# Kernel tuning notes

Measured on AMD Instinct MI355X. Metric: run time of the kernel, lower is better.

The kernel has to match this reference:

```python
import jax, jax.numpy as jnp
import numpy as np

B, S, H, E, K, F = 2, 2048, 1024, 8, 2, 4096


def setup_inputs() -> dict:
    key = jax.random.key(0)
    ks = jax.random.split(key, 6)
    scale = 0.02
    return {
        "x": jax.random.normal(ks[0], (B, S, H), dtype=jnp.float32),
        "Wg": jax.random.normal(ks[1], (H, E), dtype=jnp.float32) * scale,
        "bg": jnp.zeros((E,), dtype=jnp.float32),
        "W1": jax.random.normal(ks[2], (E, H, F), dtype=jnp.float32) * scale,  # gate proj per expert
        "W3": jax.random.normal(ks[3], (E, H, F), dtype=jnp.float32) * scale,  # up proj per expert
        "W2": jax.random.normal(ks[4], (E, F, H), dtype=jnp.float32) * scale,  # down proj per expert
    }


def reference(x, Wg, bg, W1, W3, W2):
    # --- gating: softmax -> top-k -> renormalize ---
    probs = jax.nn.softmax(jnp.einsum("bsh,he->bse", x, Wg) + bg, axis=-1)  # [B,S,E]
    topw, topi = jax.lax.top_k(probs, K)                                     # [B,S,K]
    topw = topw / jnp.sum(topw, axis=-1, keepdims=True)
    # combine weights per expert: sum over k slots of weight where index==e
    cw = jnp.sum(jax.nn.one_hot(topi, E, dtype=x.dtype) * topw[..., None], axis=-2)  # [B,S,E]

    # --- dense grouped SwiGLU experts; cw==0 zeroes out non-selected tokens,
    # which is mathematically identical to the original masked gather/scatter loop ---
    g = jnp.einsum("bsh,ehf->bsef", x, W1)            # [B,S,E,F]
    u = jnp.einsum("bsh,ehf->bsef", x, W3)            # [B,S,E,F]
    h = jax.nn.silu(g) * u                             # [B,S,E,F]
    out = jnp.einsum("bsef,efh,bse->bsh", h, W2, cw)  # weighted combine
    return out
```

## Files before the change

### kernel.cpp

```cpp
#include <hip/hip_runtime.h>
#include <hip/hip_bf16.h>
#include <math.h>

#define HD 1024
#define FD 4096
#define NE 8
#define CAP 4096

typedef __attribute__((ext_vector_type(8))) short short8;
typedef __attribute__((ext_vector_type(4))) float f32x4;

__device__ inline unsigned short f2b(float f) {
    union { float f; unsigned u; } v; v.f = f;
    unsigned r = v.u + 0x7FFF + ((v.u >> 16) & 1);
    return (unsigned short)(r >> 16);
}

__device__ inline void gll16(const void* g, void* l) {
    __builtin_amdgcn_global_load_lds(
        (const __attribute__((address_space(1))) unsigned int*)g,
        (__attribute__((address_space(3))) unsigned int*)l, 16, 0, 0);
}

__global__ __launch_bounds__(256) void convx_kernel(const float* __restrict__ x,
                                                    unsigned short* __restrict__ xbf)
{
    int i = blockIdx.x * 256 + threadIdx.x;
    float4 v = *(const float4*)(x + (size_t)i * 4);
    ushort4 b; b.x = f2b(v.x); b.y = f2b(v.y); b.z = f2b(v.z); b.w = f2b(v.w);
    *(ushort4*)(xbf + (size_t)i * 4) = b;
}

__global__ __launch_bounds__(256) void transpose_kernel(const float* __restrict__ in,
                                                        unsigned short* __restrict__ out,
                                                        int R, int C)
{
    __shared__ unsigned short Ls[64 * 72];
    int t = threadIdx.x;
    int r0 = blockIdx.x * 64, c0 = blockIdx.y * 64;
    const float* ip = in + (size_t)blockIdx.z * R * C;
    unsigned short* op = out + (size_t)blockIdx.z * (size_t)R * C;

    int rl = t >> 4, c4 = (t & 15) * 4;
#pragma unroll
    for (int p = 0; p < 4; p++) {
        int r = p * 16 + rl;
        float4 v = *(const float4*)(ip + (size_t)(r0 + r) * C + c0 + c4);
        Ls[(c4 + 0) * 72 + r] = f2b(v.x);
        Ls[(c4 + 1) * 72 + r] = f2b(v.y);
        Ls[(c4 + 2) * 72 + r] = f2b(v.z);
        Ls[(c4 + 3) * 72 + r] = f2b(v.w);
    }
    __syncthreads();
    int c = t >> 2, j2 = (t & 3) * 2;
    int orow = c0 + c;
    int blk = orow >> 7, rl2 = orow & 127;
#pragma unroll
    for (int q = 0; q < 2; q++) {
        int j = j2 + q;
        int kk = r0 + j * 8;
        uint4 v = *(const uint4*)&Ls[c * 72 + j * 8];
        size_t dst = (size_t)blk * 128 * R + (size_t)(kk >> 5) * 4096 + rl2 * 32 + (kk & 31);
        *(uint4*)(op + dst) = v;
    }
}

__global__ __launch_bounds__(256) void gate_kernel(
    const float* __restrict__ x, const float* __restrict__ Wg,
    const float* __restrict__ bg, int* __restrict__ cnt,
    int* __restrict__ btok, float* __restrict__ bw,
    int* __restrict__ tokSlot, int T)
{
    int wave = threadIdx.x >> 6;
    int lane = threadIdx.x & 63;
    int t = blockIdx.x * 4 + wave;
    if (t >= T) return;

    float part[NE];
#pragma unroll
    for (int e = 0; e < NE; e++) part[e] = 0.f;
    const float* xr = x + (size_t)t * HD;
#pragma unroll 4
    for (int j = 0; j < 16; j++) {
        int h = lane + 64 * j;
        float xv = xr[h];
        const float* wr = Wg + h * NE;
#pragma unroll
        for (int e = 0; e < NE; e++) part[e] += xv * wr[e];
    }
#pragma unroll
    for (int e = 0; e < NE; e++) {
        float v = part[e];
        for (int off = 32; off >= 1; off >>= 1) v += __shfl_xor(v, off, 64);
        part[e] = v;
    }
    if (lane == 0) {
        float lg[NE];
#pragma unroll
        for (int e = 0; e < NE; e++) lg[e] = part[e] + bg[e];
        int i0 = 0;
        for (int e = 1; e < NE; e++) if (lg[e] > lg[i0]) i0 = e;
        int i1 = -1;
        for (int e = 0; e < NE; e++) {
            if (e == i0) continue;
            if (i1 < 0 || lg[e] > lg[i1]) i1 = e;
        }
        float e1 = expf(lg[i1] - lg[i0]);
        float s = 1.0f + e1;
        float w0 = 1.0f / s, w1 = e1 / s;
        int p0 = atomicAdd(&cnt[i0], 1);
        int p1 = atomicAdd(&cnt[i1], 1);
        btok[i0 * CAP + p0] = t; bw[i0 * CAP + p0] = w0;
        btok[i1 * CAP + p1] = t; bw[i1 * CAP + p1] = w1;
        tokSlot[t * 2 + 0] = i0 * CAP + p0;
        tokSlot[t * 2 + 1] = i1 * CAP + p1;
    }
}

__global__ void scan_kernel(const int* __restrict__ cnt, int* __restrict__ offs)
{
    if (threadIdx.x == 0) {
        int acc = 0;
        for (int e = 0; e < NE; e++) { offs[e] = acc; acc += cnt[e]; }
    }
}

__global__ __launch_bounds__(256, 2) void gemm1_kernel(
    const unsigned short* __restrict__ xbf, const unsigned short* __restrict__ Wt1,
    const unsigned short* __restrict__ Wt3, const int* __restrict__ btok,
    const int* __restrict__ cnt, const int* __restrict__ offs,
    unsigned short* __restrict__ h_buf)
{
    int e = blockIdx.z;
    int ne = cnt[e];
    int m0 = blockIdx.y * 128;
    if (m0 >= ne) return;
    int f0 = blockIdx.x * 128;

    __shared__ unsigned short As[3][4096];
    __shared__ unsigned short B1s[3][4096];
    __shared__ unsigned short B3s[3][4096];

    int tid = threadIdx.x;
    int lane = tid & 63;
    int w = tid >> 6;
    int wm = (w >> 1) * 64, wn = (w & 1) * 64;
    int l15 = lane & 15, quad = lane >> 4;

    const unsigned short* W1e = Wt1 + (size_t)e * HD * FD + (size_t)blockIdx.x * (128 * HD);
    const unsigned short* W3e = Wt3 + (size_t)e * HD * FD + (size_t)blockIdx.x * (128 * HD);

    const unsigned short* aA[2];
    const unsigned short* aB1[2];
    const unsigned short* aB3[2];
    int dst[2];
#pragma unroll
    for (int q = 0; q < 2; q++) {
        int g = w * 2 + q;
        int row = g * 16 + (lane >> 2);
        int cofs = (lane & 3) * 8;
        dst[q] = g * 512;
        int ridx = m0 + row; if (ridx >= ne) ridx = ne - 1;
        int tok = btok[e * CAP + ridx];
        aA[q]  = xbf + (size_t)tok * HD + cofs;
        aB1[q] = W1e + g * 512 + lane * 8;
        aB3[q] = W3e + g * 512 + lane * 8;
    }

    int aoff[4], boff[4];
#pragma unroll
    for (int i = 0; i < 4; i++) {
        aoff[i] = (wm + i * 16 + l15) * 32 + quad * 8;
        boff[i] = (wn + i * 16 + l15) * 32 + quad * 8;
    }

    f32x4 accG[4][4], accU[4][4];
    f32x4 z = {0.f, 0.f, 0.f, 0.f};
#pragma unroll
    for (int i = 0; i < 4; i++)
#pragma unroll
        for (int jj = 0; jj < 4; jj++) { accG[i][jj] = z; accU[i][jj] = z; }

#pragma unroll
    for (int q = 0; q < 2; q++) {
        gll16(aA[q],  &As[0][dst[q]]);
        gll16(aB1[q], &B1s[0][dst[q]]);
        gll16(aB3[q], &B3s[0][dst[q]]);
    }
#pragma unroll
    for (int q = 0; q < 2; q++) {
        gll16(aA[q]  + 32,   &As[1][dst[q]]);
        gll16(aB1[q] + 4096, &B1s[1][dst[q]]);
        gll16(aB3[q] + 4096, &B3s[1][dst[q]]);
    }

    const int NK = HD / 32;
    int cur = 0;
    for (int k = 0; k < NK; ++k) {
        if (k + 2 < NK) {
            int nb = cur + 2; if (nb >= 3) nb -= 3;
#pragma unroll
            for (int q = 0; q < 2; q++) {
                gll16(aA[q]  + (k + 2) * 32,            &As[nb][dst[q]]);
                gll16(aB1[q] + (size_t)(k + 2) * 4096,  &B1s[nb][dst[q]]);
                gll16(aB3[q] + (size_t)(k + 2) * 4096,  &B3s[nb][dst[q]]);
            }
            asm volatile("s_waitcnt vmcnt(12)\ns_barrier" ::: "memory");
        } else if (k + 1 < NK) {
            asm volatile("s_waitcnt vmcnt(6)\ns_barrier" ::: "memory");
        } else {
            asm volatile("s_waitcnt vmcnt(0)\ns_barrier" ::: "memory");
        }

        __builtin_amdgcn_s_setprio(1);
        short8 af[4], b1f[4], b3f[4];
#pragma unroll
        for (int mt = 0; mt < 4; mt++) af[mt] = *(const short8*)&As[cur][aoff[mt]];
#pragma unroll
        for (int nt = 0; nt < 4; nt++) {
            b1f[nt] = *(const short8*)&B1s[cur][boff[nt]];
            b3f[nt] = *(const short8*)&B3s[cur][boff[nt]];
        }
#pragma unroll
        for (int mt = 0; mt < 4; mt++)
#pragma unroll
            for (int nt = 0; nt < 4; nt++) {
                accG[mt][nt] = __builtin_amdgcn_mfma_f32_16x16x32_bf16(af[mt], b1f[nt], accG[mt][nt], 0, 0, 0);
                accU[mt][nt] = __builtin_amdgcn_mfma_f32_16x16x32_bf16(af[mt], b3f[nt], accU[mt][nt], 0, 0, 0);
            }
        __builtin_amdgcn_s_setprio(0);
        asm volatile("s_barrier" ::: "memory");
        cur++; if (cur >= 3) cur -= 3;
    }

    int base = offs[e] + m0;
#pragma unroll
    for (int mt = 0; mt < 4; mt++) {
#pragma unroll
        for (int r = 0; r < 4; r++) {
            int rowl = wm + mt * 16 + quad * 4 + r;
            if (m0 + rowl < ne) {
                size_t rb = (size_t)(base + rowl) * FD;
#pragma unroll
                for (int nt = 0; nt < 4; nt++) {
                    int f = f0 + wn + nt * 16 + l15;
                    float g = accG[mt][nt][r];
                    float u = accU[mt][nt][r];
                    float h = g / (1.f + expf(-g)) * u;
                    h_buf[rb + f] = f2b(h);
                }
            }
        }
    }
}

__global__ __launch_bounds__(256, 3) void gemm2_kernel(
    const unsigned short* __restrict__ h_buf, const unsigned short* __restrict__ Wt2,
    const float* __restrict__ bw, const int* __restrict__ cnt,
    const int* __restrict__ offs, float* __restrict__ contrib)
{
    int e = blockIdx.z;
    int ne = cnt[e];
    int m0 = blockIdx.y * 128;
    if (m0 >= ne) return;
    int h0 = blockIdx.x * 128;

    __shared__ unsigned short As[3][4096];
    __shared__ unsigned short Bs[3][4096];

    int tid = threadIdx.x;
    int lane = tid & 63;
    int w = tid >> 6;
    int wm = (w >> 1) * 64, wn = (w & 1) * 64;
    int l15 = lane & 15, quad = lane >> 4;
    int obase = offs[e];

    const unsigned short* W2e = Wt2 + (size_t)e * FD * HD + (size_t)blockIdx.x * (128 * FD);

    const unsigned short* aA[2];
    const unsigned short* aB[2];
    int dst[2];
#pragma unroll
    for (int q = 0; q < 2; q++) {
        int g = w * 2 + q;
        int row = g * 16 + (lane >> 2);
        int cofs = (lane & 3) * 8;
        dst[q] = g * 512;
        int ridx = m0 + row; if (ridx >= ne) ridx = ne - 1;
        aA[q] = h_buf + (size_t)(obase + ridx) * FD + cofs;
        aB[q] = W2e + g * 512 + lane * 8;
    }

    int aoff[4], boff[4];
#pragma unroll
    for (int i = 0; i < 4; i++) {
        aoff[i] = (wm + i * 16 + l15) * 32 + quad * 8;
        boff[i] = (wn + i * 16 + l15) * 32 + quad * 8;
    }

    f32x4 acc[4][4];
    f32x4 z = {0.f, 0.f, 0.f, 0.f};
#pragma unroll
    for (int i = 0; i < 4; i++)
#pragma unroll
        for (int jj = 0; jj < 4; jj++) acc[i][jj] = z;

#pragma unroll
    for (int q = 0; q < 2; q++) {
        gll16(aA[q], &As[0][dst[q]]);
        gll16(aB[q], &Bs[0][dst[q]]);
    }
#pragma unroll
    for (int q = 0; q < 2; q++) {
        gll16(aA[q] + 32,   &As[1][dst[q]]);
        gll16(aB[q] + 4096, &Bs[1][dst[q]]);
    }

    const int NK = FD / 32;
    int cur = 0;
    for (int k = 0; k < NK; ++k) {
        if (k + 2 < NK) {
            int nb = cur + 2; if (nb >= 3) nb -= 3;
#pragma unroll
            for (int q = 0; q < 2; q++) {
                gll16(aA[q] + (k + 2) * 32,           &As[nb][dst[q]]);
                gll16(aB[q] + (size_t)(k + 2) * 4096, &Bs[nb][dst[q]]);
            }
            asm volatile("s_waitcnt vmcnt(8)\ns_barrier" ::: "memory");
        } else if (k + 1 < NK) {
            asm volatile("s_waitcnt vmcnt(4)\ns_barrier" ::: "memory");
        } else {
            asm volatile("s_waitcnt vmcnt(0)\ns_barrier" ::: "memory");
        }

        __builtin_amdgcn_s_setprio(1);
        short8 af[4], bf[4];
#pragma unroll
        for (int mt = 0; mt < 4; mt++) af[mt] = *(const short8*)&As[cur][aoff[mt]];
#pragma unroll
        for (int nt = 0; nt < 4; nt++) bf[nt] = *(const short8*)&Bs[cur][boff[nt]];
#pragma unroll
        for (int mt = 0; mt < 4; mt++)
#pragma unroll
            for (int nt = 0; nt < 4; nt++)
                acc[mt][nt] = __builtin_amdgcn_mfma_f32_16x16x32_bf16(af[mt], bf[nt], acc[mt][nt], 0, 0, 0);
        __builtin_amdgcn_s_setprio(0);
        asm volatile("s_barrier" ::: "memory");
        cur++; if (cur >= 3) cur -= 3;
    }

    int base = obase + m0;
#pragma unroll
    for (int mt = 0; mt < 4; mt++) {
#pragma unroll
        for (int r = 0; r < 4; r++) {
            int rowl = wm + mt * 16 + quad * 4 + r;
            if (m0 + rowl < ne) {
                float wgt = bw[e * CAP + m0 + rowl];
                size_t rb = (size_t)(base + rowl) * HD;
#pragma unroll
                for (int nt = 0; nt < 4; nt++) {
                    int col = h0 + wn + nt * 16 + l15;
                    contrib[rb + col] = acc[mt][nt][r] * wgt;
                }
            }
        }
    }
}

__global__ __launch_bounds__(256) void combine_kernel(
    const float* __restrict__ contrib, const int* __restrict__ tokSlot,
    const int* __restrict__ offs, float* __restrict__ out)
{
    int t = blockIdx.x;
    int i = threadIdx.x;
    int s0 = tokSlot[t * 2 + 0];
    int s1 = tokSlot[t * 2 + 1];
    int r0 = offs[s0 >> 12] + (s0 & (CAP - 1));
    int r1 = offs[s1 >> 12] + (s1 & (CAP - 1));
    float4 a = *(const float4*)(contrib + (size_t)r0 * HD + i * 4);
    float4 b = *(const float4*)(contrib + (size_t)r1 * HD + i * 4);
    float4 o;
    o.x = a.x + b.x; o.y = a.y + b.y; o.z = a.z + b.z; o.w = a.w + b.w;
    *(float4*)(out + (size_t)t * HD + i * 4) = o;
}

extern "C" void kernel_launch(void* const* d_in, const int* in_sizes, int n_in,
                              void* d_out, int out_size, void* d_ws, size_t ws_size,
                              hipStream_t stream)
{
    const float* x  = (const float*)d_in[0];
    const float* Wg = (const float*)d_in[1];
    const float* bg = (const float*)d_in[2];
    const float* W1 = (const float*)d_in[3];
    const float* W3 = (const float*)d_in[4];
    const float* W2 = (const float*)d_in[5];
    float* out = (float*)d_out;
    int T = in_sizes[0] / HD;

    char* ws = (char*)d_ws;
    int*   cnt     = (int*)ws;
    int*   offs    = cnt + 8;
    int*   btok    = (int*)(ws + 1024);
    float* bw      = (float*)(ws + 1024 + 131072);
    int*   tokSlot = (int*)(ws + 1024 + 262144);
    unsigned short* xbf = (unsigned short*)(ws + ((size_t)1 << 20));
    unsigned short* Wt1 = (unsigned short*)(ws + ((size_t)16 << 20));
    unsigned short* Wt3 = (unsigned short*)(ws + ((size_t)80 << 20));
    unsigned short* Wt2 = (unsigned short*)(ws + ((size_t)144 << 20));
    unsigned short* h_buf = (unsigned short*)(ws + ((size_t)208 << 20));
    float* contrib = (float*)(ws + ((size_t)272 << 20));

    hipMemsetAsync(cnt, 0, 8 * sizeof(int), stream);

    convx_kernel<<<(T * HD) / 1024, 256, 0, stream>>>(x, xbf);
    dim3 tg1(HD / 64, FD / 64, NE);
    transpose_kernel<<<tg1, 256, 0, stream>>>(W1, Wt1, HD, FD);
    transpose_kernel<<<tg1, 256, 0, stream>>>(W3, Wt3, HD, FD);
    dim3 tg2(FD / 64, HD / 64, NE);
    transpose_kernel<<<tg2, 256, 0, stream>>>(W2, Wt2, FD, HD);

    gate_kernel<<<(T + 3) / 4, 256, 0, stream>>>(x, Wg, bg, cnt, btok, bw, tokSlot, T);
    scan_kernel<<<1, 64, 0, stream>>>(cnt, offs);

    dim3 g1(FD / 128, CAP / 128, NE);
    gemm1_kernel<<<g1, 256, 0, stream>>>(xbf, Wt1, Wt3, btok, cnt, offs, h_buf);

    dim3 g2(HD / 128, CAP / 128, NE);
    gemm2_kernel<<<g2, 256, 0, stream>>>(h_buf, Wt2, bw, cnt, offs, contrib);

    combine_kernel<<<T, 256, 0, stream>>>(contrib, tokSlot, offs, out);
}
```

Measured before the change: 865.9 us.

## Swizzle LDS tiles and interleave async loads with split MFMA phases

Applies an XOR swizzle to the LDS layout of the A and B tiles in both expert GEMM kernels so that fragment reads avoid bank conflicts, with the global-load source addresses permuted to match. In the gate/up kernel the k-loop body is split into four MFMA sub-phases, and each prefetch for stage k+2 is issued between phases alongside partial fragment reads, so memory traffic overlaps compute. This adds more barriers per iteration and a more complex vmcnt accounting, which could add sync overhead or leave waits miscounted.

```diff
diff --git a/kernel.cpp b/kernel.cpp
--- a/kernel.cpp
+++ b/kernel.cpp
@@ -150,6 +150,7 @@
     const unsigned short* W1e = Wt1 + (size_t)e * HD * FD + (size_t)blockIdx.x * (128 * HD);
     const unsigned short* W3e = Wt3 + (size_t)e * HD * FD + (size_t)blockIdx.x * (128 * HD);
 
+    int swz = (((lane & 3) ^ ((lane >> 3) & 3))) * 8;
     const unsigned short* aA[2];
     const unsigned short* aB1[2];
     const unsigned short* aB3[2];
@@ -158,20 +159,21 @@
     for (int q = 0; q < 2; q++) {
         int g = w * 2 + q;
         int row = g * 16 + (lane >> 2);
-        int cofs = (lane & 3) * 8;
         dst[q] = g * 512;
         int ridx = m0 + row; if (ridx >= ne) ridx = ne - 1;
         int tok = btok[e * CAP + ridx];
-        aA[q]  = xbf + (size_t)tok * HD + cofs;
-        aB1[q] = W1e + g * 512 + lane * 8;
-        aB3[q] = W3e + g * 512 + lane * 8;
+        aA[q]  = xbf + (size_t)tok * HD + swz;
+        aB1[q] = W1e + g * 512 + (lane >> 2) * 32 + swz;
+        aB3[q] = W3e + g * 512 + (lane >> 2) * 32 + swz;
     }
 
     int aoff[4], boff[4];
 #pragma unroll
     for (int i = 0; i < 4; i++) {
-        aoff[i] = (wm + i * 16 + l15) * 32 + quad * 8;
-        boff[i] = (wn + i * 16 + l15) * 32 + quad * 8;
+        int rm = wm + i * 16 + l15;
+        aoff[i] = rm * 32 + ((quad ^ ((rm >> 1) & 3)) * 8);
+        int rn = wn + i * 16 + l15;
+        boff[i] = rn * 32 + ((quad ^ ((rn >> 1) & 3)) * 8);
     }
 
     f32x4 accG[4][4], accU[4][4];
@@ -197,39 +199,79 @@
     const int NK = HD / 32;
     int cur = 0;
     for (int k = 0; k < NK; ++k) {
-        if (k + 2 < NK) {
-            int nb = cur + 2; if (nb >= 3) nb -= 3;
-#pragma unroll
-            for (int q = 0; q < 2; q++) {
-                gll16(aA[q]  + (k + 2) * 32,            &As[nb][dst[q]]);
-                gll16(aB1[q] + (size_t)(k + 2) * 4096,  &B1s[nb][dst[q]]);
-                gll16(aB3[q] + (size_t)(k + 2) * 4096,  &B3s[nb][dst[q]]);
-            }
-            asm volatile("s_waitcnt vmcnt(12)\ns_barrier" ::: "memory");
-        } else if (k + 1 < NK) {
+        if (k + 1 < NK) {
             asm volatile("s_waitcnt vmcnt(6)\ns_barrier" ::: "memory");
         } else {
             asm volatile("s_waitcnt vmcnt(0)\ns_barrier" ::: "memory");
         }
-
+        bool st = (k + 2 < NK);
+        int nb = cur + 2; if (nb >= 3) nb -= 3;
+        int k0a = (k + 2) * 32;
+        size_t k0b = (size_t)(k + 2) * 4096;
+
+        short8 af[4], b1f[4], b3f[4];
+
+        if (st) { gll16(aA[0] + k0a, &As[nb][dst[0]]); gll16(aA[1] + k0a, &As[nb][dst[1]]); }
+        af[0] = *(const short8*)&As[cur][aoff[0]];
+        af[1] = *(const short8*)&As[cur][aoff[1]];
+        b1f[0] = *(const short8*)&B1s[cur][boff[0]];
+        b1f[1] = *(const short8*)&B1s[cur][boff[1]];
+        b3f[0] = *(const short8*)&B3s[cur][boff[0]];
+        b3f[1] = *(const short8*)&B3s[cur][boff[1]];
+        asm volatile("s_barrier" ::: "memory");
         __builtin_amdgcn_s_setprio(1);
-        short8 af[4], b1f[4], b3f[4];
-#pragma unroll
-        for (int mt = 0; mt < 4; mt++) af[mt] = *(const short8*)&As[cur][aoff[mt]];
-#pragma unroll
-        for (int nt = 0; nt < 4; nt++) {
-            b1f[nt] = *(const short8*)&B1s[cur][boff[nt]];
-            b3f[nt] = *(const short8*)&B3s[cur][boff[nt]];
-        }
-#pragma unroll
-        for (int mt = 0; mt < 4; mt++)
-#pragma unroll
-            for (int nt = 0; nt < 4; nt++) {
+#pragma unroll
+        for (int mt = 0; mt < 2; mt++)
+#pragma unroll
+            for (int nt = 0; nt < 2; nt++) {
                 accG[mt][nt] = __builtin_amdgcn_mfma_f32_16x16x32_bf16(af[mt], b1f[nt], accG[mt][nt], 0, 0, 0);
                 accU[mt][nt] = __builtin_amdgcn_mfma_f32_16x16x32_bf16(af[mt], b3f[nt], accU[mt][nt], 0, 0, 0);
             }
         __builtin_amdgcn_s_setprio(0);
         asm volatile("s_barrier" ::: "memory");
+
+        if (st) { gll16(aB1[0] + k0b, &B1s[nb][dst[0]]); gll16(aB1[1] + k0b, &B1s[nb][dst[1]]); }
+        b1f[2] = *(const short8*)&B1s[cur][boff[2]];
+        b1f[3] = *(const short8*)&B1s[cur][boff[3]];
+        b3f[2] = *(const short8*)&B3s[cur][boff[2]];
+        b3f[3] = *(const short8*)&B3s[cur][boff[3]];
+        asm volatile("s_barrier" ::: "memory");
+        __builtin_amdgcn_s_setprio(1);
+#pragma unroll
+        for (int mt = 0; mt < 2; mt++)
+#pragma unroll
+            for (int nt = 2; nt < 4; nt++) {
+                accG[mt][nt] = __builtin_amdgcn_mfma_f32_16x16x32_bf16(af[mt], b1f[nt], accG[mt][nt], 0, 0, 0);
+                accU[mt][nt] = __builtin_amdgcn_mfma_f32_16x16x32_bf16(af[mt], b3f[nt], accU[mt][nt], 0, 0, 0);
+            }
+        __builtin_amdgcn_s_setprio(0);
+        asm volatile("s_barrier" ::: "memory");
+
+        if (st) { gll16(aB3[0] + k0b, &B3s[nb][dst[0]]); gll16(aB3[1] + k0b, &B3s[nb][dst[1]]); }
+        af[2] = *(const short8*)&As[cur][aoff[2]];
+        af[3] = *(const short8*)&As[cur][aoff[3]];
+        asm volatile("s_barrier" ::: "memory");
+        __builtin_amdgcn_s_setprio(1);
+#pragma unroll
+        for (int mt = 2; mt < 4; mt++)
+#pragma unroll
+            for (int nt = 0; nt < 2; nt++) {
+                accG[mt][nt] = __builtin_amdgcn_mfma_f32_16x16x32_bf16(af[mt], b1f[nt], accG[mt][nt], 0, 0, 0);
+                accU[mt][nt] = __builtin_amdgcn_mfma_f32_16x16x32_bf16(af[mt], b3f[nt], accU[mt][nt], 0, 0, 0);
+            }
+        __builtin_amdgcn_s_setprio(0);
+        asm volatile("s_barrier" ::: "memory");
+
+        __builtin_amdgcn_s_setprio(1);
+#pragma unroll
+        for (int mt = 2; mt < 4; mt++)
+#pragma unroll
+            for (int nt = 2; nt < 4; nt++) {
+                accG[mt][nt] = __builtin_amdgcn_mfma_f32_16x16x32_bf16(af[mt], b1f[nt], accG[mt][nt], 0, 0, 0);
+                accU[mt][nt] = __builtin_amdgcn_mfma_f32_16x16x32_bf16(af[mt], b3f[nt], accU[mt][nt], 0, 0, 0);
+            }
+        __builtin_amdgcn_s_setprio(0);
+
         cur++; if (cur >= 3) cur -= 3;
     }
 
@@ -277,6 +319,7 @@
 
     const unsigned short* W2e = Wt2 + (size_t)e * FD * HD + (size_t)blockIdx.x * (128 * FD);
 
+    int swz = (((lane & 3) ^ ((lane >> 3) & 3))) * 8;
     const unsigned short* aA[2];
     const unsigned short* aB[2];
     int dst[2];
@@ -284,18 +327,19 @@
     for (int q = 0; q < 2; q++) {
         int g = w * 2 + q;
         int row = g * 16 + (lane >> 2);
-        int cofs = (lane & 3) * 8;
         dst[q] = g * 512;
         int ridx = m0 + row; if (ridx >= ne) ridx = ne - 1;
-        aA[q] = h_buf + (size_t)(obase + ridx) * FD + cofs;
-        aB[q] = W2e + g * 512 + lane * 8;
+        aA[q] = h_buf + (size_t)(obase + ridx) * FD + swz;
+        aB[q] = W2e + g * 512 + (lane >> 2) * 32 + swz;
     }
 
     int aoff[4], boff[4];
 #pragma unroll
     for (int i = 0; i < 4; i++) {
-        aoff[i] = (wm + i * 16 + l15) * 32 + quad * 8;
-        boff[i] = (wn + i * 16 + l15) * 32 + quad * 8;
+        int rm = wm + i * 16 + l15;
+        aoff[i] = rm * 32 + ((quad ^ ((rm >> 1) & 3)) * 8);
+        int rn = wn + i * 16 + l15;
+        boff[i] = rn * 32 + ((quad ^ ((rn >> 1) & 3)) * 8);
     }
 
     f32x4 acc[4][4];
```

New measurement: 908.6 us. 4.9% more time.
